# Performance work log

Hardware: AMD Instinct MI355X
Metric: run time of the kernel (lower is better)

Reference implementation:

```python
import jax, jax.numpy as jnp
import numpy as np

B, S, D = 2, 2048, 2048
H, KV, HD = 32, 8, 64  # num_heads, num_key_value_heads, head_dim
ROPE_BASE = 10000.0


def setup_inputs() -> dict:
    key = jax.random.key(0)
    k1, k2, k3 = jax.random.split(key, 3)
    x = jax.random.normal(k1, (B, S, D), dtype=jnp.float32)
    # torch Linear weights are [out_features, in_features]
    w_qkv = jax.random.normal(k2, (H * HD + 2 * KV * HD, D), dtype=jnp.float32) * (D ** -0.5)
    w_out = jax.random.normal(k3, (D, D), dtype=jnp.float32) * (D ** -0.5)
    # true RoPE tables: cos/sin are [S, HD] with the half-frequencies duplicated
    inv_freq = 1.0 / (ROPE_BASE ** (jnp.arange(0, HD, 2, dtype=jnp.float32) / HD))
    angles = jnp.arange(S, dtype=jnp.float32)[:, None] * inv_freq[None, :]  # [S, HD/2]
    emb = jnp.concatenate([angles, angles], axis=-1)  # [S, HD]
    return {"x": x, "cos": jnp.cos(emb), "sin": jnp.sin(emb), "w_qkv": w_qkv, "w_out": w_out}


def _apply_rope(t, cos, sin):
    # t: [B, h, S, HD]; cos/sin: [S, HD]
    half = t.shape[-1] // 2
    t1, t2 = t[..., :half], t[..., half:]
    rot = jnp.concatenate([-t2, t1], axis=-1)
    return t * cos[None, None, :, :] + rot * sin[None, None, :, :]


def reference(x, cos, sin, w_qkv, w_out):
    b, s, d = x.shape
    qkv = jnp.einsum('bsd,od->bso', x, w_qkv)  # merged QKV projection
    q, k, v = jnp.split(qkv, [H * HD, H * HD + KV * HD], axis=-1)
    q = q.reshape(b, s, H, HD).transpose(0, 2, 1, 3)   # [b,H,s,hd]
    k = k.reshape(b, s, KV, HD).transpose(0, 2, 1, 3)  # [b,KV,s,hd]
    v = v.reshape(b, s, KV, HD).transpose(0, 2, 1, 3)
    q = _apply_rope(q, cos, sin)
    k = _apply_rope(k, cos, sin)
    n_rep = H // KV
    k = jnp.repeat(k, n_rep, axis=1)  # repeat_kv -> [b,H,s,hd]
    v = jnp.repeat(v, n_rep, axis=1)
    scale = HD ** -0.5
    scores = jnp.einsum('bhqd,bhkd->bhqk', q, k) * scale
    causal = jnp.tril(jnp.ones((s, s), dtype=bool))
    scores = jnp.where(causal[None, None], scores, jnp.finfo(scores.dtype).min)
    attn = jax.nn.softmax(scores, axis=-1)
    out = jnp.einsum('bhqk,bhkd->bhqd', attn, v)
    out = out.transpose(0, 2, 1, 3).reshape(b, s, H * HD)
    return jnp.einsum('bso,do->bsd', out, w_out)
```

## Files before the change

kernel.cpp:

```cpp
#include <hip/hip_runtime.h>
#include <hip/hip_fp16.h>

#define B_ 2
#define S_ 2048
#define D_ 2048
#define H_ 32
#define KV_ 8
#define HD_ 64

typedef unsigned short bf16_t;
typedef __attribute__((ext_vector_type(8))) short short8;
typedef __attribute__((ext_vector_type(4))) float floatx4;
typedef __attribute__((ext_vector_type(16))) float floatx16;

__device__ __forceinline__ bf16_t f2bf(float f) {
  union { float f; unsigned u; } c; c.f = f;
  unsigned u = c.u;
  u += 0x7fffu + ((u >> 16) & 1u);
  return (bf16_t)(u >> 16);
}

__device__ __forceinline__ unsigned pk_bf16(float a, float b) {
#if __has_builtin(__builtin_amdgcn_cvt_pk_bf16_f32)
  auto v = __builtin_amdgcn_cvt_pk_bf16_f32(a, b);
  unsigned u; __builtin_memcpy(&u, &v, 4); return u;
#else
  return (unsigned)f2bf(a) | ((unsigned)f2bf(b) << 16);
#endif
}

__device__ __forceinline__ float fexp2(float x) {
#if __has_builtin(__builtin_amdgcn_exp2f)
  return __builtin_amdgcn_exp2f(x);
#else
  return exp2f(x);
#endif
}

__device__ __forceinline__ void load_lds16(const void* g, void* l) {
  __builtin_amdgcn_global_load_lds(
      (const __attribute__((address_space(1))) void*)g,
      (__attribute__((address_space(3))) void*)l, 16, 0, 0);
}

__device__ __forceinline__ void cvt4(const float* __restrict__ in,
                                     bf16_t* __restrict__ out, int i) {
  float4 v = ((const float4*)in)[i];
  ushort4 o;
  o.x = f2bf(v.x); o.y = f2bf(v.y); o.z = f2bf(v.z); o.w = f2bf(v.w);
  ((ushort4*)out)[i] = o;
}

__global__ __launch_bounds__(256) void prep(
    const float* __restrict__ x, bf16_t* __restrict__ xb,
    const float* __restrict__ wqkv, bf16_t* __restrict__ wqkvb,
    const float* __restrict__ wout, bf16_t* __restrict__ woutb,
    const float* __restrict__ cs, const float* __restrict__ sn,
    unsigned* __restrict__ tab) {
  const int bid = blockIdx.x;
  if (bid < 8192) {
    cvt4(x, xb, bid * 256 + threadIdx.x);
  } else if (bid < 14336) {
    cvt4(wqkv, wqkvb, (bid - 8192) * 256 + threadIdx.x);
  } else if (bid < 18432) {
    cvt4(wout, woutb, (bid - 14336) * 256 + threadIdx.x);
  } else {
    const int i = (bid - 18432) * 256 + threadIdx.x;
    __half2 h = __floats2half2_rn(cs[i], sn[i]);
    unsigned u; __builtin_memcpy(&u, &h, 4);
    tab[i] = u;
  }
}

__global__ __launch_bounds__(256) void gemm_bt(
    const bf16_t* __restrict__ A, const bf16_t* __restrict__ Bm,
    float* __restrict__ C, int M, int N, int K) {
  __shared__ __attribute__((aligned(16))) bf16_t As[128 * 32];
  __shared__ __attribute__((aligned(16))) bf16_t Bs[128 * 32];
  const int tid = threadIdx.x;
  const int lane = tid & 63;
  const int wave = tid >> 6;
  const int bm = blockIdx.y * 128, bn = blockIdx.x * 128;
  const int wm = (wave >> 1) * 64, wn = (wave & 1) * 64;
  const int lr = lane & 15, quad = lane >> 4;

  floatx4 acc[4][4] = {};

  const int t0 = tid, t1 = tid + 256;
  const int r0 = t0 >> 2, c0 = (t0 & 3) * 8;
  const int r1 = t1 >> 2, c1 = (t1 & 3) * 8;

  const bf16_t* Ab = A + (size_t)bm * K;
  const bf16_t* Bb = Bm + (size_t)bn * K;

  for (int k0 = 0; k0 < K; k0 += 32) {
    __syncthreads();
    load_lds16(Ab + (size_t)r0 * K + k0 + c0, &As[t0 * 8]);
    load_lds16(Ab + (size_t)r1 * K + k0 + c1, &As[t1 * 8]);
    load_lds16(Bb + (size_t)r0 * K + k0 + c0, &Bs[t0 * 8]);
    load_lds16(Bb + (size_t)r1 * K + k0 + c1, &Bs[t1 * 8]);
    __syncthreads();

    short8 af[4], bfr[4];
#pragma unroll
    for (int i = 0; i < 4; i++) {
      af[i]  = *(const short8*)&As[(wm + i * 16 + lr) * 32 + quad * 8];
      bfr[i] = *(const short8*)&Bs[(wn + i * 16 + lr) * 32 + quad * 8];
    }
#pragma unroll
    for (int mi = 0; mi < 4; mi++)
#pragma unroll
      for (int ni = 0; ni < 4; ni++)
        acc[mi][ni] = __builtin_amdgcn_mfma_f32_16x16x32_bf16(af[mi], bfr[ni], acc[mi][ni], 0, 0, 0);
  }

#pragma unroll
  for (int mi = 0; mi < 4; mi++) {
    const int row = bm + wm + mi * 16 + quad * 4;
#pragma unroll
    for (int ni = 0; ni < 4; ni++) {
      const int col = bn + wn + ni * 16 + lr;
      float* cp = C + (size_t)row * N + col;
#pragma unroll
      for (int r = 0; r < 4; r++) cp[(size_t)r * N] = acc[mi][ni][r];
    }
  }
}

__global__ __launch_bounds__(256, 4) void gemm_qkv(
    const bf16_t* __restrict__ A, const bf16_t* __restrict__ Bm,
    const unsigned* __restrict__ tab,
    bf16_t* __restrict__ q, bf16_t* __restrict__ k, bf16_t* __restrict__ vt) {
  const int K = 2048;
  __shared__ __attribute__((aligned(16))) bf16_t As[128 * 32];
  __shared__ __attribute__((aligned(16))) bf16_t Bs[128 * 32];
  __shared__ __attribute__((aligned(16))) bf16_t Ts[4][32 * 72];
  const int tid = threadIdx.x;
  const int lane = tid & 63;
  const int wave = tid >> 6;
  const int bm = blockIdx.y * 128, bn = blockIdx.x * 128;
  const int wm = (wave >> 1) * 64, wn = (wave & 1) * 64;
  const int lr = lane & 15, quad = lane >> 4;

  floatx4 acc[4][4] = {};

  const int t0 = tid, t1 = tid + 256;
  const int r0 = t0 >> 2, c0 = (t0 & 3) * 8;
  const int r1 = t1 >> 2, c1 = (t1 & 3) * 8;

  const bf16_t* Ab = A + (size_t)bm * K;
  const bf16_t* Bb = Bm + (size_t)bn * K;

  for (int k0 = 0; k0 < K; k0 += 32) {
    __syncthreads();
    load_lds16(Ab + (size_t)r0 * K + k0 + c0, &As[t0 * 8]);
    load_lds16(Ab + (size_t)r1 * K + k0 + c1, &As[t1 * 8]);
    load_lds16(Bb + (size_t)r0 * K + k0 + c0, &Bs[t0 * 8]);
    load_lds16(Bb + (size_t)r1 * K + k0 + c1, &Bs[t1 * 8]);
    __syncthreads();

    short8 af[4], bfr[4];
#pragma unroll
    for (int i = 0; i < 4; i++) {
      af[i]  = *(const short8*)&As[(wm + i * 16 + lr) * 32 + quad * 8];
      bfr[i] = *(const short8*)&Bs[(wn + i * 16 + lr) * 32 + quad * 8];
    }
#pragma unroll
    for (int mi = 0; mi < 4; mi++)
#pragma unroll
      for (int ni = 0; ni < 4; ni++)
        acc[mi][ni] = __builtin_amdgcn_mfma_f32_16x16x32_bf16(af[mi], bfr[ni], acc[mi][ni], 0, 0, 0);
  }

  const int f0 = bn + wn;
  const int srow0 = bm + wm;
  const int bb = srow0 >> 11, s0 = srow0 & 2047;

  if (f0 < 2560) {
    const bool isq = (f0 < 2048);
    const float scale = isq ? 0.18033688011f : 1.0f;
    bf16_t* dst = isq ? (q + (size_t)(bb * H_ + (f0 >> 6)) * S_ * HD_)
                      : (k + (size_t)(bb * KV_ + ((f0 - 2048) >> 6)) * S_ * HD_);
#pragma unroll
    for (int mi = 0; mi < 4; mi++) {
#pragma unroll
      for (int r = 0; r < 4; r++) {
        const int sr = s0 + mi * 16 + quad * 4 + r;
        const unsigned* tp = tab + (size_t)sr * HD_;
        bf16_t* drow = dst + (size_t)sr * HD_;
#pragma unroll
        for (int ni = 0; ni < 4; ni++) {
          const int d = ni * 16 + lr;
          const unsigned w = tp[d];
          __half2 h2; __builtin_memcpy(&h2, &w, 4);
          const float2 cf = __half22float2(h2);
          const float t = acc[mi][ni][r];
          const float oth = acc[mi][ni ^ 2][r];
          const float rot = (ni < 2) ? -oth : oth;
          drow[d] = f2bf((t * cf.x + rot * cf.y) * scale);
        }
      }
    }
  } else {
    const int hv = (f0 - 2560) >> 6;
    bf16_t* ts = Ts[wave];
    const int rl = lane >> 1, hf = lane & 1;
#pragma unroll
    for (int p = 0; p < 2; p++) {
#pragma unroll
      for (int nn = 0; nn < 2; nn++) {
        const int ni = 2 * p + nn;
#pragma unroll
        for (int mi = 0; mi < 4; mi++) {
          uint2 pw;
          pw.x = pk_bf16(acc[mi][ni][0], acc[mi][ni][1]);
          pw.y = pk_bf16(acc[mi][ni][2], acc[mi][ni][3]);
          *(uint2*)&ts[(nn * 16 + lr) * 72 + mi * 16 + quad * 4] = pw;
        }
      }
      bf16_t* vrow = vt + ((size_t)(bb * KV_ + hv) * HD_ + p * 32 + rl) * S_ + s0 + hf * 32;
#pragma unroll
      for (int j = 0; j < 4; j++)
        *(short8*)(vrow + j * 8) = *(const short8*)&ts[rl * 72 + hf * 32 + j * 8];
    }
  }
}


__device__ __forceinline__ void stage64x2(const bf16_t* __restrict__ g, int rstride,
                                          bf16_t* lbuf, int wave, int lane) {
  const int sub = lane >> 3;
  const int sc  = lane & 7;
  const int gc  = sc ^ sub;
#pragma unroll
  for (int j = 0; j < 4; j++) {
    const int r = wave * 32 + j * 8 + sub;
    load_lds16(g + (size_t)r * rstride + gc * 8,
               lbuf + (wave * 256 + j * 64 + lane) * 8);
  }
}

__device__ __forceinline__ void hswap(unsigned a, unsigned b, unsigned& x, unsigned& y) {
#if __has_builtin(__builtin_amdgcn_permlane32_swap)
  auto r = __builtin_amdgcn_permlane32_swap(a, b, false, false);
  x = (unsigned)r[0]; y = (unsigned)r[1];
#else
  const unsigned pa = (unsigned)__shfl_xor((int)a, 32, 64);
  const unsigned pb = (unsigned)__shfl_xor((int)b, 32, 64);
  const bool hi = (threadIdx.x & 32) != 0;
  x = hi ? pb : a;
  y = hi ? b : pa;
#endif
}

__device__ __forceinline__ void build_pfrag(const floatx16& p, short8& f0, short8& f1) {
  unsigned w[8];
  const unsigned c01 = pk_bf16(p[0], p[1]);
  const unsigned c45 = pk_bf16(p[4], p[5]);
  const unsigned c23 = pk_bf16(p[2], p[3]);
  const unsigned c67 = pk_bf16(p[6], p[7]);
  hswap(c01, c45, w[0], w[2]);
  hswap(c23, c67, w[1], w[3]);
  const unsigned d01 = pk_bf16(p[8], p[9]);
  const unsigned d45 = pk_bf16(p[12], p[13]);
  const unsigned d23 = pk_bf16(p[10], p[11]);
  const unsigned d67 = pk_bf16(p[14], p[15]);
  hswap(d01, d45, w[4], w[6]);
  hswap(d23, d67, w[5], w[7]);
  __builtin_memcpy(&f0, &w[0], 16);
  __builtin_memcpy(&f1, &w[4], 16);
}

__device__ __forceinline__ void attn_half32(
    const bf16_t* __restrict__ Q, const bf16_t* __restrict__ kb,
    const bf16_t* __restrict__ vb, bf16_t* __restrict__ O,
    bf16_t* Ks, bf16_t* Vs, int b, int h, int bh, int T, int wave, int lane) {
  const int nt = T + 1;
  const int q0 = T * 64 + wave * 32;
  const int cq = lane & 31;
  const int hh = lane >> 5;
  const int sw7 = lane & 7;

  const bf16_t* qp = Q + ((size_t)bh * S_ + q0 + cq) * HD_ + hh * 8;
  short8 qf[4];
#pragma unroll
  for (int ds = 0; ds < 4; ds++) qf[ds] = *(const short8*)(qp + ds * 16);

  floatx16 o0 = {}, o1 = {};
  float m = -1e30f, l = 0.f;

  stage64x2(kb, HD_, Ks, wave, lane);
  stage64x2(vb, S_, Vs, wave, lane);

  for (int kt = 0; kt < nt; kt++) {
    __syncthreads();
    if (kt + 1 < nt) {
      stage64x2(kb + (size_t)(kt + 1) * 64 * HD_, HD_, Ks + ((kt + 1) & 1) * 4096, wave, lane);
      stage64x2(vb + (kt + 1) * 64, S_, Vs + ((kt + 1) & 1) * 4096, wave, lane);
    }
    const bf16_t* Kc = Ks + (kt & 1) * 4096;
    const bf16_t* Vc = Vs + (kt & 1) * 4096;

    floatx16 s0 = {}, s1 = {};
    __builtin_amdgcn_s_setprio(1);
#pragma unroll
    for (int ds = 0; ds < 4; ds++) {
      const int slot = (((ds * 2 + hh) ^ sw7) * 8);
      const short8 k0 = *(const short8*)&Kc[cq * 64 + slot];
      const short8 k1 = *(const short8*)&Kc[(32 + cq) * 64 + slot];
      s0 = __builtin_amdgcn_mfma_f32_32x32x16_bf16(k0, qf[ds], s0, 0, 0, 0);
      s1 = __builtin_amdgcn_mfma_f32_32x32x16_bf16(k1, qf[ds], s1, 0, 0, 0);
    }
    __builtin_amdgcn_s_setprio(0);

    if (kt == T) {
      const int qg = q0 + cq;
      const int kbase = kt * 64 + 4 * hh;
#pragma unroll
      for (int r = 0; r < 16; r++) {
        const int kg = kbase + (r & 3) + 8 * (r >> 2);
        s0[r] = (kg <= qg) ? s0[r] : -1e30f;
        s1[r] = (kg + 32 <= qg) ? s1[r] : -1e30f;
      }
    }

    float t[8];
#pragma unroll
    for (int i = 0; i < 8; i++)
      t[i] = fmaxf(fmaxf(s0[i], s0[i + 8]), fmaxf(s1[i], s1[i + 8]));
#pragma unroll
    for (int st = 4; st >= 1; st >>= 1)
#pragma unroll
      for (int i = 0; i < st; i++) t[i] = fmaxf(t[i], t[i + st]);
    float mx = t[0];
    mx = fmaxf(mx, __shfl_xor(mx, 32, 64));

    if (!__all(mx <= m + 8.0f)) {
      const float mn = fmaxf(m, mx);
      const float a = fexp2(m - mn);
      l *= a;
#pragma unroll
      for (int i = 0; i < 16; i++) { o0[i] *= a; o1[i] *= a; }
      m = mn;
    }

#pragma unroll
    for (int i = 0; i < 16; i++) {
      s0[i] = fexp2(s0[i] - m);
      s1[i] = fexp2(s1[i] - m);
    }
    float u[8];
#pragma unroll
    for (int i = 0; i < 8; i++)
      u[i] = (s0[i] + s0[i + 8]) + (s1[i] + s1[i + 8]);
#pragma unroll
    for (int st = 4; st >= 1; st >>= 1)
#pragma unroll
      for (int i = 0; i < st; i++) u[i] += u[i + st];
    l += u[0];

    short8 pf[4];
    build_pfrag(s0, pf[0], pf[1]);
    build_pfrag(s1, pf[2], pf[3]);

    __builtin_amdgcn_s_setprio(1);
#pragma unroll
    for (int ks = 0; ks < 4; ks++) {
      const int slot = (((ks * 2 + hh) ^ sw7) * 8);
      const short8 v0 = *(const short8*)&Vc[cq * 64 + slot];
      const short8 v1 = *(const short8*)&Vc[(32 + cq) * 64 + slot];
      o0 = __builtin_amdgcn_mfma_f32_32x32x16_bf16(v0, pf[ks], o0, 0, 0, 0);
      o1 = __builtin_amdgcn_mfma_f32_32x32x16_bf16(v1, pf[ks], o1, 0, 0, 0);
    }
    __builtin_amdgcn_s_setprio(0);
  }

  const float lt = l + __shfl_xor(l, 32, 64);
  const float li = 1.f / lt;
  bf16_t* ob = O + ((size_t)b * S_ + q0 + cq) * (H_ * HD_) + h * HD_ + hh * 4;
#pragma unroll
  for (int rq = 0; rq < 4; rq++) {
    uint2 w0;
    w0.x = pk_bf16(o0[4 * rq] * li, o0[4 * rq + 1] * li);
    w0.y = pk_bf16(o0[4 * rq + 2] * li, o0[4 * rq + 3] * li);
    *(uint2*)(ob + rq * 8) = w0;
    uint2 w1;
    w1.x = pk_bf16(o1[4 * rq] * li, o1[4 * rq + 1] * li);
    w1.y = pk_bf16(o1[4 * rq + 2] * li, o1[4 * rq + 3] * li);
    *(uint2*)(ob + 32 + rq * 8) = w1;
  }
}

__global__ __launch_bounds__(128, 2) void flash_attn(
    const bf16_t* __restrict__ Q,
    const bf16_t* __restrict__ Kc,
    const bf16_t* __restrict__ Vt,
    bf16_t* __restrict__ O) {
  __shared__ __attribute__((aligned(16))) bf16_t Ks[2 * 4096];
  __shared__ __attribute__((aligned(16))) bf16_t Vs[2 * 4096];
  const int bh = blockIdx.y;
  const int b = bh >> 5, h = bh & 31;
  const int kvh = b * KV_ + (h >> 2);
  const int wave = threadIdx.x >> 6, lane = threadIdx.x & 63;

  const bf16_t* kb = Kc + (size_t)kvh * S_ * HD_;
  const bf16_t* vb = Vt + (size_t)kvh * HD_ * S_;

  const int ta = blockIdx.x;
  const int tb = 31 - blockIdx.x;
  attn_half32(Q, kb, vb, O, Ks, Vs, b, h, bh, ta, wave, lane);
  __syncthreads();
  attn_half32(Q, kb, vb, O, Ks, Vs, b, h, bh, tb, wave, lane);
}

extern "C" void kernel_launch(void* const* d_in, const int* in_sizes, int n_in,
                              void* d_out, int out_size, void* d_ws, size_t ws_size,
                              hipStream_t stream) {
  const float* x    = (const float*)d_in[0];
  const float* cs   = (const float*)d_in[1];
  const float* sn   = (const float*)d_in[2];
  const float* wqkv = (const float*)d_in[3];
  const float* wout = (const float*)d_in[4];
  float* out = (float*)d_out;

  char* ws = (char*)d_ws;
  bf16_t*  xb    = (bf16_t*)(ws);
  bf16_t*  wqkvb = (bf16_t*)(ws + 16777216);
  bf16_t*  woutb = (bf16_t*)(ws + 29360128);
  bf16_t*  qb    = (bf16_t*)(ws + 37748736);
  bf16_t*  kb    = (bf16_t*)(ws + 54525952);
  bf16_t*  vtb   = (bf16_t*)(ws + 58720256);
  bf16_t*  attnb = (bf16_t*)(ws + 62914560);
  unsigned* tab  = (unsigned*)(ws + 79691776);

  prep<<<18944, 256, 0, stream>>>(x, xb, wqkv, wqkvb, wout, woutb, cs, sn, tab);
  gemm_qkv<<<dim3(24, 32), 256, 0, stream>>>(xb, wqkvb, tab, qb, kb, vtb);
  flash_attn<<<dim3(16, 64), 128, 0, stream>>>(qb, kb, vtb, attnb);
  gemm_bt<<<dim3(16, 32), 256, 0, stream>>>(attnb, woutb, out, 4096, 2048, 2048);
}
```

Before: 305.7 us.

## Use 32-key attention tiles with per-wave causal skip and one q-tile per block

The flash attention kernel now stages 32-key K/V tiles instead of 64-key tiles, halving shared memory and raising launch bounds to 4 blocks per SM. Each block handles a single 64-query tile, scheduled in reverse order, so the grid doubles and the paired-tile load balancing is dropped. Each wave skips key tiles past its own causal diagonal, which removes the masked half-tile of work on the diagonal. In exchange there are more loop iterations, more barriers per key processed, and smaller MFMA batches per softmax step.

```diff
diff --git a/kernel.cpp b/kernel.cpp
--- a/kernel.cpp
+++ b/kernel.cpp
@@ -227,16 +227,23 @@
 }
 
 
-__device__ __forceinline__ void stage64x2(const bf16_t* __restrict__ g, int rstride,
-                                          bf16_t* lbuf, int wave, int lane) {
-  const int sub = lane >> 3;
-  const int sc  = lane & 7;
-  const int gc  = sc ^ sub;
-#pragma unroll
-  for (int j = 0; j < 4; j++) {
-    const int r = wave * 32 + j * 8 + sub;
-    load_lds16(g + (size_t)r * rstride + gc * 8,
-               lbuf + (wave * 256 + j * 64 + lane) * 8);
+__device__ __forceinline__ void stage32(const bf16_t* __restrict__ gk,
+                                        const bf16_t* __restrict__ gv,
+                                        bf16_t* kbuf, bf16_t* vbuf,
+                                        int wave, int lane) {
+#pragma unroll
+  for (int j = 0; j < 2; j++) {
+    const int r = wave * 16 + j * 8 + (lane >> 3);
+    const int gc = (lane & 7) ^ (r & 7);
+    load_lds16(gk + (size_t)r * HD_ + gc * 8,
+               kbuf + wave * 1024 + j * 512 + lane * 8);
+  }
+#pragma unroll
+  for (int j = 0; j < 2; j++) {
+    const int r = wave * 32 + j * 16 + (lane >> 2);
+    const int gc = (lane & 3) ^ ((r >> 1) & 3);
+    load_lds16(gv + (size_t)r * S_ + gc * 8,
+               vbuf + wave * 1024 + j * 512 + lane * 8);
   }
 }
 
@@ -271,16 +278,25 @@
   __builtin_memcpy(&f1, &w[4], 16);
 }
 
-__device__ __forceinline__ void attn_half32(
-    const bf16_t* __restrict__ Q, const bf16_t* __restrict__ kb,
-    const bf16_t* __restrict__ vb, bf16_t* __restrict__ O,
-    bf16_t* Ks, bf16_t* Vs, int b, int h, int bh, int T, int wave, int lane) {
-  const int nt = T + 1;
+__global__ __launch_bounds__(128, 4) void flash_attn(
+    const bf16_t* __restrict__ Q,
+    const bf16_t* __restrict__ Kc,
+    const bf16_t* __restrict__ Vt,
+    bf16_t* __restrict__ O) {
+  __shared__ __attribute__((aligned(16))) bf16_t Ks[2 * 2048];
+  __shared__ __attribute__((aligned(16))) bf16_t Vs[2 * 2048];
+  const int bh = blockIdx.y;
+  const int b = bh >> 5, h = bh & 31;
+  const int kvh = b * KV_ + (h >> 2);
+  const int wave = threadIdx.x >> 6, lane = threadIdx.x & 63;
+  const int T = 31 - blockIdx.x;
+  const int cq = lane & 31, hh = lane >> 5;
+
+  const bf16_t* kb = Kc + (size_t)kvh * S_ * HD_;
+  const bf16_t* vb = Vt + (size_t)kvh * HD_ * S_;
+
   const int q0 = T * 64 + wave * 32;
-  const int cq = lane & 31;
-  const int hh = lane >> 5;
-  const int sw7 = lane & 7;
-
+  const int qg = q0 + cq;
   const bf16_t* qp = Q + ((size_t)bh * S_ + q0 + cq) * HD_ + hh * 8;
   short8 qf[4];
 #pragma unroll
@@ -289,51 +305,47 @@
   floatx16 o0 = {}, o1 = {};
   float m = -1e30f, l = 0.f;
 
-  stage64x2(kb, HD_, Ks, wave, lane);
-  stage64x2(vb, S_, Vs, wave, lane);
+  const int nt = 2 * T + 2;
+  const int last = 2 * T + wave;
+
+  stage32(kb, vb, Ks, Vs, wave, lane);
 
   for (int kt = 0; kt < nt; kt++) {
     __syncthreads();
-    if (kt + 1 < nt) {
-      stage64x2(kb + (size_t)(kt + 1) * 64 * HD_, HD_, Ks + ((kt + 1) & 1) * 4096, wave, lane);
-      stage64x2(vb + (kt + 1) * 64, S_, Vs + ((kt + 1) & 1) * 4096, wave, lane);
-    }
-    const bf16_t* Kc = Ks + (kt & 1) * 4096;
-    const bf16_t* Vc = Vs + (kt & 1) * 4096;
-
-    floatx16 s0 = {}, s1 = {};
+    if (kt + 1 < nt)
+      stage32(kb + (size_t)(kt + 1) * 32 * HD_, vb + (kt + 1) * 32,
+              Ks + ((kt + 1) & 1) * 2048, Vs + ((kt + 1) & 1) * 2048, wave, lane);
+    if (kt > last) continue;
+    const bf16_t* Kt = Ks + (kt & 1) * 2048;
+    const bf16_t* Vc = Vs + (kt & 1) * 2048;
+
+    floatx16 s = {};
     __builtin_amdgcn_s_setprio(1);
 #pragma unroll
     for (int ds = 0; ds < 4; ds++) {
-      const int slot = (((ds * 2 + hh) ^ sw7) * 8);
-      const short8 k0 = *(const short8*)&Kc[cq * 64 + slot];
-      const short8 k1 = *(const short8*)&Kc[(32 + cq) * 64 + slot];
-      s0 = __builtin_amdgcn_mfma_f32_32x32x16_bf16(k0, qf[ds], s0, 0, 0, 0);
-      s1 = __builtin_amdgcn_mfma_f32_32x32x16_bf16(k1, qf[ds], s1, 0, 0, 0);
+      const int c = ds * 2 + hh;
+      const short8 kf = *(const short8*)&Kt[cq * 64 + ((c ^ (cq & 7)) * 8)];
+      s = __builtin_amdgcn_mfma_f32_32x32x16_bf16(kf, qf[ds], s, 0, 0, 0);
     }
     __builtin_amdgcn_s_setprio(0);
 
-    if (kt == T) {
-      const int qg = q0 + cq;
-      const int kbase = kt * 64 + 4 * hh;
+    if (kt == last) {
+      const int kb0 = kt * 32 + 4 * hh;
 #pragma unroll
       for (int r = 0; r < 16; r++) {
-        const int kg = kbase + (r & 3) + 8 * (r >> 2);
-        s0[r] = (kg <= qg) ? s0[r] : -1e30f;
-        s1[r] = (kg + 32 <= qg) ? s1[r] : -1e30f;
+        const int kg = kb0 + (r & 3) + 8 * (r >> 2);
+        s[r] = (kg <= qg) ? s[r] : -1e30f;
       }
     }
 
     float t[8];
 #pragma unroll
-    for (int i = 0; i < 8; i++)
-      t[i] = fmaxf(fmaxf(s0[i], s0[i + 8]), fmaxf(s1[i], s1[i + 8]));
+    for (int i = 0; i < 8; i++) t[i] = fmaxf(s[i], s[i + 8]);
 #pragma unroll
     for (int st = 4; st >= 1; st >>= 1)
 #pragma unroll
       for (int i = 0; i < st; i++) t[i] = fmaxf(t[i], t[i + st]);
-    float mx = t[0];
-    mx = fmaxf(mx, __shfl_xor(mx, 32, 64));
+    float mx = fmaxf(t[0], __shfl_xor(t[0], 32, 64));
 
     if (!__all(mx <= m + 8.0f)) {
       const float mn = fmaxf(m, mx);
@@ -345,30 +357,26 @@
     }
 
 #pragma unroll
-    for (int i = 0; i < 16; i++) {
-      s0[i] = fexp2(s0[i] - m);
-      s1[i] = fexp2(s1[i] - m);
-    }
+    for (int i = 0; i < 16; i++) s[i] = fexp2(s[i] - m);
     float u[8];
 #pragma unroll
-    for (int i = 0; i < 8; i++)
-      u[i] = (s0[i] + s0[i + 8]) + (s1[i] + s1[i + 8]);
+    for (int i = 0; i < 8; i++) u[i] = s[i] + s[i + 8];
 #pragma unroll
     for (int st = 4; st >= 1; st >>= 1)
 #pragma unroll
       for (int i = 0; i < st; i++) u[i] += u[i + st];
     l += u[0];
 
-    short8 pf[4];
-    build_pfrag(s0, pf[0], pf[1]);
-    build_pfrag(s1, pf[2], pf[3]);
+    short8 pf[2];
+    build_pfrag(s, pf[0], pf[1]);
 
     __builtin_amdgcn_s_setprio(1);
 #pragma unroll
-    for (int ks = 0; ks < 4; ks++) {
-      const int slot = (((ks * 2 + hh) ^ sw7) * 8);
-      const short8 v0 = *(const short8*)&Vc[cq * 64 + slot];
-      const short8 v1 = *(const short8*)&Vc[(32 + cq) * 64 + slot];
+    for (int ks = 0; ks < 2; ks++) {
+      const int c = ks * 2 + hh;
+      const int sv = (c ^ ((cq >> 1) & 3)) * 8;
+      const short8 v0 = *(const short8*)&Vc[cq * 32 + sv];
+      const short8 v1 = *(const short8*)&Vc[(32 + cq) * 32 + sv];
       o0 = __builtin_amdgcn_mfma_f32_32x32x16_bf16(v0, pf[ks], o0, 0, 0, 0);
       o1 = __builtin_amdgcn_mfma_f32_32x32x16_bf16(v1, pf[ks], o1, 0, 0, 0);
     }
@@ -377,40 +385,18 @@
 
   const float lt = l + __shfl_xor(l, 32, 64);
   const float li = 1.f / lt;
-  bf16_t* ob = O + ((size_t)b * S_ + q0 + cq) * (H_ * HD_) + h * HD_ + hh * 4;
+  bf16_t* obp = O + ((size_t)b * S_ + q0 + cq) * (H_ * HD_) + h * HD_ + hh * 4;
 #pragma unroll
   for (int rq = 0; rq < 4; rq++) {
     uint2 w0;
     w0.x = pk_bf16(o0[4 * rq] * li, o0[4 * rq + 1] * li);
     w0.y = pk_bf16(o0[4 * rq + 2] * li, o0[4 * rq + 3] * li);
-    *(uint2*)(ob + rq * 8) = w0;
+    *(uint2*)(obp + rq * 8) = w0;
     uint2 w1;
     w1.x = pk_bf16(o1[4 * rq] * li, o1[4 * rq + 1] * li);
     w1.y = pk_bf16(o1[4 * rq + 2] * li, o1[4 * rq + 3] * li);
-    *(uint2*)(ob + 32 + rq * 8) = w1;
-  }
-}
-
-__global__ __launch_bounds__(128, 2) void flash_attn(
-    const bf16_t* __restrict__ Q,
-    const bf16_t* __restrict__ Kc,
-    const bf16_t* __restrict__ Vt,
-    bf16_t* __restrict__ O) {
-  __shared__ __attribute__((aligned(16))) bf16_t Ks[2 * 4096];
-  __shared__ __attribute__((aligned(16))) bf16_t Vs[2 * 4096];
-  const int bh = blockIdx.y;
-  const int b = bh >> 5, h = bh & 31;
-  const int kvh = b * KV_ + (h >> 2);
-  const int wave = threadIdx.x >> 6, lane = threadIdx.x & 63;
-
-  const bf16_t* kb = Kc + (size_t)kvh * S_ * HD_;
-  const bf16_t* vb = Vt + (size_t)kvh * HD_ * S_;
-
-  const int ta = blockIdx.x;
-  const int tb = 31 - blockIdx.x;
-  attn_half32(Q, kb, vb, O, Ks, Vs, b, h, bh, ta, wave, lane);
-  __syncthreads();
-  attn_half32(Q, kb, vb, O, Ks, Vs, b, h, bh, tb, wave, lane);
+    *(uint2*)(obp + 32 + rq * 8) = w1;
+  }
 }
 
 extern "C" void kernel_launch(void* const* d_in, const int* in_sizes, int n_in,
@@ -435,6 +421,6 @@
 
   prep<<<18944, 256, 0, stream>>>(x, xb, wqkv, wqkvb, wout, woutb, cs, sn, tab);
   gemm_qkv<<<dim3(24, 32), 256, 0, stream>>>(xb, wqkvb, tab, qb, kb, vtb);
-  flash_attn<<<dim3(16, 64), 128, 0, stream>>>(qb, kb, vtb, attnb);
+  flash_attn<<<dim3(32, 64), 128, 0, stream>>>(qb, kb, vtb, attnb);
   gemm_bt<<<dim3(16, 32), 256, 0, stream>>>(attnb, woutb, out, 4096, 2048, 2048);
 }
```

New measurement: 352.5 us. 1.15x slower.

## Deepen GEMM K-tile to 64 with XOR-swizzled LDS and widen attention blocks

Applied to the files above, without the earlier changes.

Both GEMMs now stage a 128x64 K-slice per iteration into XOR-swizzled LDS and run two MFMA sub-steps per barrier pair. This halves the number of barriers and should reduce LDS bank conflicts. The flash attention kernel changes from 128-thread blocks, each handling two 64-query tiles paired for causal balance, to 256-thread blocks that each cover a 128-query tile. Blocks are launched longest-first with a head-interleaved order so K/V staging is shared across four waves. The cost is more LDS per GEMM block, and in attention some waves idle on the final key tile while the others finish.

```diff
diff --git a/kernel.cpp b/kernel.cpp
--- a/kernel.cpp
+++ b/kernel.cpp
@@ -75,8 +75,8 @@
 __global__ __launch_bounds__(256) void gemm_bt(
     const bf16_t* __restrict__ A, const bf16_t* __restrict__ Bm,
     float* __restrict__ C, int M, int N, int K) {
-  __shared__ __attribute__((aligned(16))) bf16_t As[128 * 32];
-  __shared__ __attribute__((aligned(16))) bf16_t Bs[128 * 32];
+  __shared__ __attribute__((aligned(16))) bf16_t As[128 * 64];
+  __shared__ __attribute__((aligned(16))) bf16_t Bs[128 * 64];
   const int tid = threadIdx.x;
   const int lane = tid & 63;
   const int wave = tid >> 6;
@@ -86,32 +86,37 @@
 
   floatx4 acc[4][4] = {};
 
-  const int t0 = tid, t1 = tid + 256;
-  const int r0 = t0 >> 2, c0 = (t0 & 3) * 8;
-  const int r1 = t1 >> 2, c1 = (t1 & 3) * 8;
-
   const bf16_t* Ab = A + (size_t)bm * K;
   const bf16_t* Bb = Bm + (size_t)bn * K;
 
-  for (int k0 = 0; k0 < K; k0 += 32) {
+  for (int k0 = 0; k0 < K; k0 += 64) {
     __syncthreads();
-    load_lds16(Ab + (size_t)r0 * K + k0 + c0, &As[t0 * 8]);
-    load_lds16(Ab + (size_t)r1 * K + k0 + c1, &As[t1 * 8]);
-    load_lds16(Bb + (size_t)r0 * K + k0 + c0, &Bs[t0 * 8]);
-    load_lds16(Bb + (size_t)r1 * K + k0 + c1, &Bs[t1 * 8]);
+#pragma unroll
+    for (int p = 0; p < 4; p++) {
+      const int idx = p * 256 + tid;
+      const int row = idx >> 3, sc = idx & 7;
+      const int gc = sc ^ (row & 7);
+      load_lds16(Ab + (size_t)row * K + k0 + gc * 8, &As[idx * 8]);
+      load_lds16(Bb + (size_t)row * K + k0 + gc * 8, &Bs[idx * 8]);
+    }
     __syncthreads();
 
-    short8 af[4], bfr[4];
-#pragma unroll
-    for (int i = 0; i < 4; i++) {
-      af[i]  = *(const short8*)&As[(wm + i * 16 + lr) * 32 + quad * 8];
-      bfr[i] = *(const short8*)&Bs[(wn + i * 16 + lr) * 32 + quad * 8];
-    }
-#pragma unroll
-    for (int mi = 0; mi < 4; mi++)
-#pragma unroll
-      for (int ni = 0; ni < 4; ni++)
-        acc[mi][ni] = __builtin_amdgcn_mfma_f32_16x16x32_bf16(af[mi], bfr[ni], acc[mi][ni], 0, 0, 0);
+#pragma unroll
+    for (int ks = 0; ks < 2; ks++) {
+      short8 af[4], bfr[4];
+#pragma unroll
+      for (int i = 0; i < 4; i++) {
+        const int ra = wm + i * 16 + lr;
+        const int rb = wn + i * 16 + lr;
+        af[i]  = *(const short8*)&As[ra * 64 + (((ks * 4 + quad) ^ (ra & 7)) * 8)];
+        bfr[i] = *(const short8*)&Bs[rb * 64 + (((ks * 4 + quad) ^ (rb & 7)) * 8)];
+      }
+#pragma unroll
+      for (int mi = 0; mi < 4; mi++)
+#pragma unroll
+        for (int ni = 0; ni < 4; ni++)
+          acc[mi][ni] = __builtin_amdgcn_mfma_f32_16x16x32_bf16(af[mi], bfr[ni], acc[mi][ni], 0, 0, 0);
+    }
   }
 
 #pragma unroll
@@ -132,8 +137,8 @@
     const unsigned* __restrict__ tab,
     bf16_t* __restrict__ q, bf16_t* __restrict__ k, bf16_t* __restrict__ vt) {
   const int K = 2048;
-  __shared__ __attribute__((aligned(16))) bf16_t As[128 * 32];
-  __shared__ __attribute__((aligned(16))) bf16_t Bs[128 * 32];
+  __shared__ __attribute__((aligned(16))) bf16_t As[128 * 64];
+  __shared__ __attribute__((aligned(16))) bf16_t Bs[128 * 64];
   __shared__ __attribute__((aligned(16))) bf16_t Ts[4][32 * 72];
   const int tid = threadIdx.x;
   const int lane = tid & 63;
@@ -144,32 +149,37 @@
 
   floatx4 acc[4][4] = {};
 
-  const int t0 = tid, t1 = tid + 256;
-  const int r0 = t0 >> 2, c0 = (t0 & 3) * 8;
-  const int r1 = t1 >> 2, c1 = (t1 & 3) * 8;
-
   const bf16_t* Ab = A + (size_t)bm * K;
   const bf16_t* Bb = Bm + (size_t)bn * K;
 
-  for (int k0 = 0; k0 < K; k0 += 32) {
+  for (int k0 = 0; k0 < K; k0 += 64) {
     __syncthreads();
-    load_lds16(Ab + (size_t)r0 * K + k0 + c0, &As[t0 * 8]);
-    load_lds16(Ab + (size_t)r1 * K + k0 + c1, &As[t1 * 8]);
-    load_lds16(Bb + (size_t)r0 * K + k0 + c0, &Bs[t0 * 8]);
-    load_lds16(Bb + (size_t)r1 * K + k0 + c1, &Bs[t1 * 8]);
+#pragma unroll
+    for (int p = 0; p < 4; p++) {
+      const int idx = p * 256 + tid;
+      const int row = idx >> 3, sc = idx & 7;
+      const int gc = sc ^ (row & 7);
+      load_lds16(Ab + (size_t)row * K + k0 + gc * 8, &As[idx * 8]);
+      load_lds16(Bb + (size_t)row * K + k0 + gc * 8, &Bs[idx * 8]);
+    }
     __syncthreads();
 
-    short8 af[4], bfr[4];
-#pragma unroll
-    for (int i = 0; i < 4; i++) {
-      af[i]  = *(const short8*)&As[(wm + i * 16 + lr) * 32 + quad * 8];
-      bfr[i] = *(const short8*)&Bs[(wn + i * 16 + lr) * 32 + quad * 8];
-    }
-#pragma unroll
-    for (int mi = 0; mi < 4; mi++)
-#pragma unroll
-      for (int ni = 0; ni < 4; ni++)
-        acc[mi][ni] = __builtin_amdgcn_mfma_f32_16x16x32_bf16(af[mi], bfr[ni], acc[mi][ni], 0, 0, 0);
+#pragma unroll
+    for (int ks = 0; ks < 2; ks++) {
+      short8 af[4], bfr[4];
+#pragma unroll
+      for (int i = 0; i < 4; i++) {
+        const int ra = wm + i * 16 + lr;
+        const int rb = wn + i * 16 + lr;
+        af[i]  = *(const short8*)&As[ra * 64 + (((ks * 4 + quad) ^ (ra & 7)) * 8)];
+        bfr[i] = *(const short8*)&Bs[rb * 64 + (((ks * 4 + quad) ^ (rb & 7)) * 8)];
+      }
+#pragma unroll
+      for (int mi = 0; mi < 4; mi++)
+#pragma unroll
+        for (int ni = 0; ni < 4; ni++)
+          acc[mi][ni] = __builtin_amdgcn_mfma_f32_16x16x32_bf16(af[mi], bfr[ni], acc[mi][ni], 0, 0, 0);
+    }
   }
 
   const int f0 = bn + wn;
@@ -227,16 +237,17 @@
 }
 
 
-__device__ __forceinline__ void stage64x2(const bf16_t* __restrict__ g, int rstride,
-                                          bf16_t* lbuf, int wave, int lane) {
-  const int sub = lane >> 3;
-  const int sc  = lane & 7;
-  const int gc  = sc ^ sub;
-#pragma unroll
-  for (int j = 0; j < 4; j++) {
-    const int r = wave * 32 + j * 8 + sub;
-    load_lds16(g + (size_t)r * rstride + gc * 8,
-               lbuf + (wave * 256 + j * 64 + lane) * 8);
+__device__ __forceinline__ void stage64_4w(const bf16_t* __restrict__ gk,
+                                           const bf16_t* __restrict__ gv,
+                                           bf16_t* kbuf, bf16_t* vbuf, int tid) {
+#pragma unroll
+  for (int j = 0; j < 2; j++) {
+    const int idx = j * 256 + tid;
+    const int row = idx >> 3;
+    const int sc  = idx & 7;
+    const int gc  = sc ^ (row & 7);
+    load_lds16(gk + (size_t)row * HD_ + gc * 8, kbuf + idx * 8);
+    load_lds16(gv + (size_t)row * S_  + gc * 8, vbuf + idx * 8);
   }
 }
 
@@ -271,17 +282,30 @@
   __builtin_memcpy(&f1, &w[4], 16);
 }
 
-__device__ __forceinline__ void attn_half32(
-    const bf16_t* __restrict__ Q, const bf16_t* __restrict__ kb,
-    const bf16_t* __restrict__ vb, bf16_t* __restrict__ O,
-    bf16_t* Ks, bf16_t* Vs, int b, int h, int bh, int T, int wave, int lane) {
-  const int nt = T + 1;
-  const int q0 = T * 64 + wave * 32;
-  const int cq = lane & 31;
-  const int hh = lane >> 5;
+__global__ __launch_bounds__(256, 2) void flash_attn(
+    const bf16_t* __restrict__ Q,
+    const bf16_t* __restrict__ Kc,
+    const bf16_t* __restrict__ Vt,
+    bf16_t* __restrict__ O) {
+  __shared__ __attribute__((aligned(16))) bf16_t Ks[2 * 4096];
+  __shared__ __attribute__((aligned(16))) bf16_t Vs[2 * 4096];
+  const int bid = blockIdx.x;
+  const int head = ((bid & 7) << 3) | ((bid >> 3) & 7);
+  const int Tb = 15 - (bid >> 6);
+  const int b = head >> 5, h = head & 31;
+  const int kvh = b * KV_ + (h >> 2);
+  const int tid = threadIdx.x;
+  const int wave = tid >> 6, lane = tid & 63;
+  const int cq = lane & 31, hh = lane >> 5;
   const int sw7 = lane & 7;
-
-  const bf16_t* qp = Q + ((size_t)bh * S_ + q0 + cq) * HD_ + hh * 8;
+  const int q0 = Tb * 128 + wave * 32, qg = q0 + cq;
+  const int nt = 2 * Tb + 2;
+  const int last = 2 * Tb + (wave >> 1);
+
+  const bf16_t* kb = Kc + (size_t)kvh * S_ * HD_;
+  const bf16_t* vb = Vt + (size_t)kvh * HD_ * S_;
+
+  const bf16_t* qp = Q + ((size_t)head * S_ + qg) * HD_ + hh * 8;
   short8 qf[4];
 #pragma unroll
   for (int ds = 0; ds < 4; ds++) qf[ds] = *(const short8*)(qp + ds * 16);
@@ -289,16 +313,15 @@
   floatx16 o0 = {}, o1 = {};
   float m = -1e30f, l = 0.f;
 
-  stage64x2(kb, HD_, Ks, wave, lane);
-  stage64x2(vb, S_, Vs, wave, lane);
+  stage64_4w(kb, vb, Ks, Vs, tid);
 
   for (int kt = 0; kt < nt; kt++) {
     __syncthreads();
-    if (kt + 1 < nt) {
-      stage64x2(kb + (size_t)(kt + 1) * 64 * HD_, HD_, Ks + ((kt + 1) & 1) * 4096, wave, lane);
-      stage64x2(vb + (kt + 1) * 64, S_, Vs + ((kt + 1) & 1) * 4096, wave, lane);
-    }
-    const bf16_t* Kc = Ks + (kt & 1) * 4096;
+    if (kt + 1 < nt)
+      stage64_4w(kb + (size_t)(kt + 1) * 64 * HD_, vb + (kt + 1) * 64,
+                 Ks + ((kt + 1) & 1) * 4096, Vs + ((kt + 1) & 1) * 4096, tid);
+    if (kt > last) continue;
+    const bf16_t* Kt = Ks + (kt & 1) * 4096;
     const bf16_t* Vc = Vs + (kt & 1) * 4096;
 
     floatx16 s0 = {}, s1 = {};
@@ -306,15 +329,14 @@
 #pragma unroll
     for (int ds = 0; ds < 4; ds++) {
       const int slot = (((ds * 2 + hh) ^ sw7) * 8);
-      const short8 k0 = *(const short8*)&Kc[cq * 64 + slot];
-      const short8 k1 = *(const short8*)&Kc[(32 + cq) * 64 + slot];
+      const short8 k0 = *(const short8*)&Kt[cq * 64 + slot];
+      const short8 k1 = *(const short8*)&Kt[(32 + cq) * 64 + slot];
       s0 = __builtin_amdgcn_mfma_f32_32x32x16_bf16(k0, qf[ds], s0, 0, 0, 0);
       s1 = __builtin_amdgcn_mfma_f32_32x32x16_bf16(k1, qf[ds], s1, 0, 0, 0);
     }
     __builtin_amdgcn_s_setprio(0);
 
-    if (kt == T) {
-      const int qg = q0 + cq;
+    if (kt == last) {
       const int kbase = kt * 64 + 4 * hh;
 #pragma unroll
       for (int r = 0; r < 16; r++) {
@@ -377,40 +399,18 @@
 
   const float lt = l + __shfl_xor(l, 32, 64);
   const float li = 1.f / lt;
-  bf16_t* ob = O + ((size_t)b * S_ + q0 + cq) * (H_ * HD_) + h * HD_ + hh * 4;
+  bf16_t* obp = O + ((size_t)b * S_ + qg) * (H_ * HD_) + h * HD_ + hh * 4;
 #pragma unroll
   for (int rq = 0; rq < 4; rq++) {
     uint2 w0;
     w0.x = pk_bf16(o0[4 * rq] * li, o0[4 * rq + 1] * li);
     w0.y = pk_bf16(o0[4 * rq + 2] * li, o0[4 * rq + 3] * li);
-    *(uint2*)(ob + rq * 8) = w0;
+    *(uint2*)(obp + rq * 8) = w0;
     uint2 w1;
     w1.x = pk_bf16(o1[4 * rq] * li, o1[4 * rq + 1] * li);
     w1.y = pk_bf16(o1[4 * rq + 2] * li, o1[4 * rq + 3] * li);
-    *(uint2*)(ob + 32 + rq * 8) = w1;
-  }
-}
-
-__global__ __launch_bounds__(128, 2) void flash_attn(
-    const bf16_t* __restrict__ Q,
-    const bf16_t* __restrict__ Kc,
-    const bf16_t* __restrict__ Vt,
-    bf16_t* __restrict__ O) {
-  __shared__ __attribute__((aligned(16))) bf16_t Ks[2 * 4096];
-  __shared__ __attribute__((aligned(16))) bf16_t Vs[2 * 4096];
-  const int bh = blockIdx.y;
-  const int b = bh >> 5, h = bh & 31;
-  const int kvh = b * KV_ + (h >> 2);
-  const int wave = threadIdx.x >> 6, lane = threadIdx.x & 63;
-
-  const bf16_t* kb = Kc + (size_t)kvh * S_ * HD_;
-  const bf16_t* vb = Vt + (size_t)kvh * HD_ * S_;
-
-  const int ta = blockIdx.x;
-  const int tb = 31 - blockIdx.x;
-  attn_half32(Q, kb, vb, O, Ks, Vs, b, h, bh, ta, wave, lane);
-  __syncthreads();
-  attn_half32(Q, kb, vb, O, Ks, Vs, b, h, bh, tb, wave, lane);
+    *(uint2*)(obp + 32 + rq * 8) = w1;
+  }
 }
 
 extern "C" void kernel_launch(void* const* d_in, const int* in_sizes, int n_in,
@@ -435,6 +435,6 @@
 
   prep<<<18944, 256, 0, stream>>>(x, xb, wqkv, wqkvb, wout, woutb, cs, sn, tab);
   gemm_qkv<<<dim3(24, 32), 256, 0, stream>>>(xb, wqkvb, tab, qb, kb, vtb);
-  flash_attn<<<dim3(16, 64), 128, 0, stream>>>(qb, kb, vtb, attnb);
+  flash_attn<<<1024, 256, 0, stream>>>(qb, kb, vtb, attnb);
   gemm_bt<<<dim3(16, 32), 256, 0, stream>>>(attnb, woutb, out, 4096, 2048, 2048);
 }
```

After: 292.1 us. 1.05x faster.
